# Optimization experiments

Measured on AMD Instinct MI355X. Metric: run time of the kernel, lower is better.

Reference implementation:

```python
import jax, jax.numpy as jnp
import numpy as np

EPS = 1e-5

def instance_norm(x):
    # x: [B, C, H, W]; normalize over spatial dims per (b, c), no affine
    mean = jnp.mean(x, axis=(2, 3), keepdims=True)
    var = jnp.var(x, axis=(2, 3), keepdims=True)
    return (x - mean) * jax.lax.rsqrt(var + EPS)

def conv1x1(x, w, b):
    # x: [B, Cin, H, W], w: [Cout, Cin], b: [Cout]
    return jnp.einsum('bchw,oc->bohw', x, w) + b[None, :, None, None]

def setup_inputs() -> dict:
    key = jax.random.key(0)
    k1, k2, k3 = jax.random.split(key, 3)
    B, Cin, Cout, H, W = 16, 256, 256, 128, 128
    x = jax.random.normal(k1, (B, Cin, H, W), dtype=jnp.float32)
    # PyTorch Conv2d init: U(-s, s), s = 1/sqrt(fan_in) with fan_in = Cin*1*1
    s1 = 1.0 / np.sqrt(Cin)
    w1 = jax.random.uniform(k2, (Cout, Cin), jnp.float32, -s1, s1)
    b1 = jax.random.uniform(jax.random.fold_in(k2, 1), (Cout,), jnp.float32, -s1, s1)
    s2 = 1.0 / np.sqrt(Cout)
    w2 = jax.random.uniform(k3, (Cout, Cout), jnp.float32, -s2, s2)
    b2 = jax.random.uniform(jax.random.fold_in(k3, 1), (Cout,), jnp.float32, -s2, s2)
    return {"x": x, "w1": w1, "b1": b1, "w2": w2, "b2": b2}

def reference(x, w1, b1, w2, b2):
    h = jax.nn.relu(conv1x1(instance_norm(x), w1, b1))
    out = jax.nn.relu(conv1x1(instance_norm(h), w2, b2))
    return out
```

## Files before the change

### kernel.cpp

```cpp
#include <hip/hip_runtime.h>
#include <hip/hip_bf16.h>
#include <cstdint>
#include <cstddef>

#define DEVI __device__ __forceinline__

typedef unsigned short u16;
using frag_ab = __attribute__((ext_vector_type(8))) short;
using f32x4   = __attribute__((ext_vector_type(4))) float;

constexpr int HW = 16384;
constexpr int NC = 256;

DEVI u16 bf16bits(float f) {
    union { float f; uint32_t u; } cv; cv.f = f;
    uint32_t u = cv.u;
    u += 0x7fffu + ((u >> 16) & 1u);
    return (u16)(u >> 16);
}

DEVI void gload16(const void* g, void* l) {
    __builtin_amdgcn_global_load_lds(
        (const __attribute__((address_space(1))) uint32_t*)g,
        (__attribute__((address_space(3))) uint32_t*)l, 16, 0, 0);
}

DEVI frag_ab read_frag(const u16* slab, int row, int l4) {
    const int phys = (l4 ^ row ^ (row >> 2)) & 3;
    return *(const frag_ab*)((const char*)slab + row * 64 + phys * 16);
}

__global__ __launch_bounds__(256) void transpose_stats_kernel(
    const float* __restrict__ x, u16* __restrict__ xt,
    float* __restrict__ ps, float* __restrict__ pq)
{
    constexpr int PADW = 68;
    __shared__ __align__(16) u16 tile[64 * PADW];
    const int b = blockIdx.z, c0 = blockIdx.y * 64, p0 = blockIdx.x * 64;
    const int pblk = blockIdx.x;
    const int t = threadIdx.x;
    const int lane = t & 63, w = t >> 6;
    const int pq_ = lane & 15, cq = lane >> 4;
    const int quad = w * 4 + cq;
    const float* xb = x + ((size_t)b * NC + c0) * HW + p0;

    float va[4][4];
    float aS[4], aQ[4];
    #pragma unroll
    for (int j = 0; j < 4; ++j) {
        const float4 v = *(const float4*)(xb + (size_t)(quad * 4 + j) * HW + pq_ * 4);
        va[j][0] = v.x; va[j][1] = v.y; va[j][2] = v.z; va[j][3] = v.w;
        float s1 = v.x + v.y + v.z + v.w;
        float s2 = v.x*v.x + v.y*v.y + v.z*v.z + v.w*v.w;
        #pragma unroll
        for (int d = 1; d < 16; d <<= 1) {
            s1 += __shfl_xor(s1, d, 64);
            s2 += __shfl_xor(s2, d, 64);
        }
        aS[j] = s1; aQ[j] = s2;
    }
    if (pq_ == 0) {
        const float4 vs = {aS[0], aS[1], aS[2], aS[3]};
        const float4 vq = {aQ[0], aQ[1], aQ[2], aQ[3]};
        *(float4*)&ps[((size_t)b * 256 + pblk) * NC + c0 + quad * 4] = vs;
        *(float4*)&pq[((size_t)b * 256 + pblk) * NC + c0 + quad * 4] = vq;
    }
    #pragma unroll
    for (int i = 0; i < 4; ++i) {
        alignas(8) u16 pk[4];
        #pragma unroll
        for (int j = 0; j < 4; ++j) pk[j] = bf16bits(va[j][i]);
        *(uint2*)&tile[(pq_ * 4 + i) * PADW + quad * 4] = *(const uint2*)pk;
    }
    __syncthreads();
    const int pl = t >> 2, q = t & 3;
    u16* dst = xt + ((size_t)b * HW + p0 + pl) * NC + c0;
    #pragma unroll
    for (int s = 0; s < 2; ++s) {
        const int ch8 = q + s * 4;
        const uint2 lo = *(const uint2*)&tile[pl * PADW + ch8 * 8];
        const uint2 hi = *(const uint2*)&tile[pl * PADW + ch8 * 8 + 4];
        const uint4 o4 = {lo.x, lo.y, hi.x, hi.y};
        *(uint4*)(dst + ch8 * 8) = o4;
    }
}

__global__ __launch_bounds__(256) void fold_kernel(
    const float* __restrict__ w, const float* __restrict__ bias,
    const float* __restrict__ ps, const float* __restrict__ pq,
    u16* __restrict__ we, float* __restrict__ be)
{
    const int b = blockIdx.y, oc = blockIdx.x * 64;
    __shared__ float mu[NC], rs[NC];
    __shared__ __align__(16) float wt[64 * NC];
    const int t = threadIdx.x;
    {
        float s1 = 0.f, s2 = 0.f;
        const float* pp = ps + (size_t)b * 256 * NC + t;
        const float* qq = pq + (size_t)b * 256 * NC + t;
        for (int i = 0; i < 256; ++i) {
            s1 += pp[(size_t)i * NC];
            s2 += qq[(size_t)i * NC];
        }
        const float m = s1 * (1.0f / HW);
        mu[t] = m;
        rs[t] = rsqrtf(s2 * (1.0f / HW) - m * m + 1e-5f);
    }
    #pragma unroll
    for (int i = 0; i < 16; ++i)
        *(float4*)&wt[i*1024 + t*4] = *(const float4*)&w[(size_t)oc*NC + i*1024 + t*4];
    __syncthreads();
    const int o = oc + (t >> 2), q = t & 3;
    const float* wrow = &wt[(t >> 2) * NC];
    u16* werow = we + ((size_t)b * NC + o) * NC;
    float bacc = 0.f;
    for (int cc = 0; cc < 8; ++cc) {
        alignas(16) u16 pk[8];
        #pragma unroll
        for (int jj = 0; jj < 8; ++jj) {
            const int c = q*64 + cc*8 + jj;
            const float wv = wrow[c];
            bacc -= wv * mu[c] * rs[c];
            pk[jj] = bf16bits(wv * rs[c]);
        }
        *(uint4*)(werow + q*64 + cc*8) = *(const uint4*)pk;
    }
    bacc += __shfl_xor(bacc, 1, 64);
    bacc += __shfl_xor(bacc, 2, 64);
    if (q == 0) be[b*NC + o] = bias[o] + bacc;
}

template<int STAGE>
__global__ __launch_bounds__(256, 2) void gemm_kernel(
    const u16* __restrict__ pixM,
    const u16* __restrict__ wMat,
    const float* __restrict__ biasE,
    u16* __restrict__ outB,
    float* __restrict__ outF,
    float* __restrict__ hps, float* __restrict__ hpq)
{
    __shared__ __align__(16) u16 ldsP[8 * 64 * 32];
    __shared__ __align__(16) u16 ldsW[2][256 * 32];

    const int b = blockIdx.y, pblk = blockIdx.x;
    const int p0 = pblk * 64;
    const int tid = threadIdx.x;
    const int lane = tid & 63, wid = tid >> 6;
    const int l15 = lane & 15, l4 = lane >> 4;

    const u16* gP = pixM + ((size_t)b * HW + p0) * NC;
    const u16* gW = wMat + (size_t)b * NC * NC;

    const int rin  = lane >> 2;
    const int prow = wid * 16 + rin;
    const int psl  = ((lane & 3) ^ prow ^ (prow >> 2)) & 3;
    int wrowq[4], wslq[4];
    #pragma unroll
    for (int q = 0; q < 4; ++q) {
        wrowq[q] = wid * 64 + q * 16 + rin;
        wslq[q]  = ((lane & 3) ^ wrowq[q] ^ (wrowq[q] >> 2)) & 3;
    }

    #pragma unroll
    for (int ks = 0; ks < 8; ++ks)
        gload16(gP + (size_t)prow * NC + ks * 32 + psl * 8,
                (char*)ldsP + ks * 4096 + wid * 1024);
    #pragma unroll
    for (int q = 0; q < 4; ++q)
        gload16(gW + (size_t)wrowq[q] * NC + wslq[q] * 8,
                (char*)ldsW[0] + (wid * 4 + q) * 1024);

    f32x4 acc[4][4];
    #pragma unroll
    for (int i = 0; i < 4; ++i)
        #pragma unroll
        for (int j = 0; j < 4; ++j)
            acc[i][j] = (f32x4){0.f, 0.f, 0.f, 0.f};

    for (int ks = 0; ks < 8; ++ks) {
        asm volatile("s_waitcnt vmcnt(0)" ::: "memory");
        __builtin_amdgcn_s_barrier();

        const u16* wslab = ldsW[ks & 1];
        const u16* pslab = ldsP + ks * 2048;

        const u16* sA; const u16* sB; int aOff, bOff;
        if constexpr (STAGE == 1) { sA = pslab; aOff = 0;        sB = wslab; bOff = wid * 64; }
        else                      { sA = wslab; aOff = wid * 64; sB = pslab; bOff = 0; }

        frag_ab a[4], bf[4];
        #pragma unroll
        for (int mi = 0; mi < 4; ++mi)
            a[mi] = read_frag(sA, aOff + 16*mi + l15, l4);
        #pragma unroll
        for (int ni = 0; ni < 4; ++ni)
            bf[ni] = read_frag(sB, bOff + 16*ni + l15, l4);

        if (ks < 7) {
            const int k0 = (ks + 1) * 32;
            #pragma unroll
            for (int q = 0; q < 4; ++q)
                gload16(gW + (size_t)wrowq[q] * NC + k0 + wslq[q] * 8,
                        (char*)ldsW[(ks + 1) & 1] + (wid * 4 + q) * 1024);
        }

        #pragma unroll
        for (int ni = 0; ni < 4; ++ni)
            #pragma unroll
            for (int mi = 0; mi < 4; ++mi)
                acc[mi][ni] = __builtin_amdgcn_mfma_f32_16x16x32_bf16(a[mi], bf[ni], acc[mi][ni], 0, 0, 0);
    }

    if constexpr (STAGE == 1) {
        u16* htp = outB + ((size_t)b * HW + p0) * NC + wid * 64;
        float s1[4] = {0.f,0.f,0.f,0.f}, s2[4] = {0.f,0.f,0.f,0.f};
        #pragma unroll
        for (int ni = 0; ni < 4; ++ni) {
            const float bn = biasE[b*NC + wid*64 + 16*ni + l15];
            #pragma unroll
            for (int mi = 0; mi < 4; ++mi) {
                #pragma unroll
                for (int r = 0; r < 4; ++r) {
                    const float v = fmaxf(acc[mi][ni][r] + bn, 0.f);
                    s1[ni] += v; s2[ni] += v * v;
                    htp[(size_t)(16*mi + l4*4 + r) * NC + 16*ni + l15] = bf16bits(v);
                }
            }
        }
        #pragma unroll
        for (int ni = 0; ni < 4; ++ni) {
            float a1 = s1[ni], a2 = s2[ni];
            a1 += __shfl_xor(a1, 16, 64); a1 += __shfl_xor(a1, 32, 64);
            a2 += __shfl_xor(a2, 16, 64); a2 += __shfl_xor(a2, 32, 64);
            if (l4 == 0) {
                const int col = wid*64 + 16*ni + l15;
                hps[((size_t)b * 256 + pblk) * NC + col] = a1;
                hpq[((size_t)b * 256 + pblk) * NC + col] = a2;
            }
        }
    } else {
        float* op = outF + ((size_t)b * NC + wid * 64) * HW + p0;
        #pragma unroll
        for (int mi = 0; mi < 4; ++mi) {
            #pragma unroll
            for (int r = 0; r < 4; ++r) {
                const int orow = 16*mi + l4*4 + r;
                const float bm = biasE[b*NC + wid*64 + orow];
                #pragma unroll
                for (int ni = 0; ni < 4; ++ni)
                    op[(size_t)orow * HW + 16*ni + l15] = fmaxf(acc[mi][ni][r] + bm, 0.f);
            }
        }
    }
}

extern "C" void kernel_launch(void* const* d_in, const int* in_sizes, int n_in,
                              void* d_out, int out_size, void* d_ws, size_t ws_size,
                              hipStream_t stream)
{
    (void)in_sizes; (void)n_in; (void)out_size;
    const float* x  = (const float*)d_in[0];
    const float* w1 = (const float*)d_in[1];
    const float* b1 = (const float*)d_in[2];
    const float* w2 = (const float*)d_in[3];
    const float* b2 = (const float*)d_in[4];
    float* out = (float*)d_out;

    char* od = (char*)d_out;
    u16*   xt  = (u16*)od;
    float* xps = (float*)(od + 134217728);
    float* xpq = (float*)(od + 138412032);
    float* hps = (float*)(od + 142606336);
    float* hpq = (float*)(od + 146800640);

    char* ws = (char*)d_ws;
    const size_t NEED = 138444800;
    if (ws_size < NEED) return;
    u16*   ht  = (u16*)(ws);
    u16*   w1e = (u16*)(ws + 134217728);
    u16*   w2e = (u16*)(ws + 136314880);
    float* b1e = (float*)(ws + 138412032);
    float* b2e = (float*)(ws + 138428416);

    transpose_stats_kernel<<<dim3(HW/64, NC/64, 16), 256, 0, stream>>>(x, xt, xps, xpq);
    fold_kernel<<<dim3(4, 16), 256, 0, stream>>>(w1, b1, xps, xpq, w1e, b1e);
    gemm_kernel<1><<<dim3(HW/64, 16), 256, 0, stream>>>(xt, w1e, b1e, ht, nullptr, hps, hpq);
    fold_kernel<<<dim3(4, 16), 256, 0, stream>>>(w2, b2, hps, hpq, w2e, b2e);
    gemm_kernel<2><<<dim3(HW/64, 16), 256, 0, stream>>>(ht, w2e, b2e, nullptr, out, nullptr, nullptr);
}
```

Before: 315.8 us.

## Load weight fragments directly to registers, drop LDS weight buffer, add nontemporal stores

```diff
diff --git a/kernel.cpp b/kernel.cpp
--- a/kernel.cpp
+++ b/kernel.cpp
@@ -8,6 +8,7 @@
 typedef unsigned short u16;
 using frag_ab = __attribute__((ext_vector_type(8))) short;
 using f32x4   = __attribute__((ext_vector_type(4))) float;
+using u32x4   = __attribute__((ext_vector_type(4))) unsigned int;
 
 constexpr int HW = 16384;
 constexpr int NC = 256;
@@ -80,8 +81,8 @@
         const int ch8 = q + s * 4;
         const uint2 lo = *(const uint2*)&tile[pl * PADW + ch8 * 8];
         const uint2 hi = *(const uint2*)&tile[pl * PADW + ch8 * 8 + 4];
-        const uint4 o4 = {lo.x, lo.y, hi.x, hi.y};
-        *(uint4*)(dst + ch8 * 8) = o4;
+        const u32x4 o4 = {lo.x, lo.y, hi.x, hi.y};
+        __builtin_nontemporal_store(o4, (u32x4*)(dst + ch8 * 8));
     }
 }
 
@@ -131,7 +132,7 @@
 }
 
 template<int STAGE>
-__global__ __launch_bounds__(256, 2) void gemm_kernel(
+__global__ __launch_bounds__(256, 3) void gemm_kernel(
     const u16* __restrict__ pixM,
     const u16* __restrict__ wMat,
     const float* __restrict__ biasE,
@@ -140,7 +141,6 @@
     float* __restrict__ hps, float* __restrict__ hpq)
 {
     __shared__ __align__(16) u16 ldsP[8 * 64 * 32];
-    __shared__ __align__(16) u16 ldsW[2][256 * 32];
 
     const int b = blockIdx.y, pblk = blockIdx.x;
     const int p0 = pblk * 64;
@@ -154,21 +154,13 @@
     const int rin  = lane >> 2;
     const int prow = wid * 16 + rin;
     const int psl  = ((lane & 3) ^ prow ^ (prow >> 2)) & 3;
-    int wrowq[4], wslq[4];
-    #pragma unroll
-    for (int q = 0; q < 4; ++q) {
-        wrowq[q] = wid * 64 + q * 16 + rin;
-        wslq[q]  = ((lane & 3) ^ wrowq[q] ^ (wrowq[q] >> 2)) & 3;
-    }
 
     #pragma unroll
     for (int ks = 0; ks < 8; ++ks)
         gload16(gP + (size_t)prow * NC + ks * 32 + psl * 8,
                 (char*)ldsP + ks * 4096 + wid * 1024);
-    #pragma unroll
-    for (int q = 0; q < 4; ++q)
-        gload16(gW + (size_t)wrowq[q] * NC + wslq[q] * 8,
-                (char*)ldsW[0] + (wid * 4 + q) * 1024);
+
+    const u16* wbase = gW + (size_t)(wid * 64 + l15) * NC + l4 * 8;
 
     f32x4 acc[4][4];
     #pragma unroll
@@ -177,38 +169,37 @@
         for (int j = 0; j < 4; ++j)
             acc[i][j] = (f32x4){0.f, 0.f, 0.f, 0.f};
 
+    frag_ab wf[2][4];
+    #pragma unroll
+    for (int f = 0; f < 4; ++f)
+        wf[0][f] = *(const frag_ab*)(wbase + (size_t)f * 16 * NC);
+
+    asm volatile("s_waitcnt vmcnt(0)" ::: "memory");
+    __builtin_amdgcn_s_barrier();
+
+    #pragma unroll
     for (int ks = 0; ks < 8; ++ks) {
-        asm volatile("s_waitcnt vmcnt(0)" ::: "memory");
-        __builtin_amdgcn_s_barrier();
-
-        const u16* wslab = ldsW[ks & 1];
+        const int cur = ks & 1;
+        if (ks < 7) {
+            #pragma unroll
+            for (int f = 0; f < 4; ++f)
+                wf[cur ^ 1][f] = *(const frag_ab*)(wbase + (size_t)f * 16 * NC + (ks + 1) * 32);
+        }
         const u16* pslab = ldsP + ks * 2048;
-
-        const u16* sA; const u16* sB; int aOff, bOff;
-        if constexpr (STAGE == 1) { sA = pslab; aOff = 0;        sB = wslab; bOff = wid * 64; }
-        else                      { sA = wslab; aOff = wid * 64; sB = pslab; bOff = 0; }
-
-        frag_ab a[4], bf[4];
-        #pragma unroll
-        for (int mi = 0; mi < 4; ++mi)
-            a[mi] = read_frag(sA, aOff + 16*mi + l15, l4);
+        frag_ab pf[4];
+        #pragma unroll
+        for (int f = 0; f < 4; ++f)
+            pf[f] = read_frag(pslab, 16 * f + l15, l4);
+
         #pragma unroll
         for (int ni = 0; ni < 4; ++ni)
-            bf[ni] = read_frag(sB, bOff + 16*ni + l15, l4);
-
-        if (ks < 7) {
-            const int k0 = (ks + 1) * 32;
-            #pragma unroll
-            for (int q = 0; q < 4; ++q)
-                gload16(gW + (size_t)wrowq[q] * NC + k0 + wslq[q] * 8,
-                        (char*)ldsW[(ks + 1) & 1] + (wid * 4 + q) * 1024);
-        }
-
-        #pragma unroll
-        for (int ni = 0; ni < 4; ++ni)
-            #pragma unroll
-            for (int mi = 0; mi < 4; ++mi)
-                acc[mi][ni] = __builtin_amdgcn_mfma_f32_16x16x32_bf16(a[mi], bf[ni], acc[mi][ni], 0, 0, 0);
+            #pragma unroll
+            for (int mi = 0; mi < 4; ++mi) {
+                if constexpr (STAGE == 1)
+                    acc[mi][ni] = __builtin_amdgcn_mfma_f32_16x16x32_bf16(pf[mi], wf[cur][ni], acc[mi][ni], 0, 0, 0);
+                else
+                    acc[mi][ni] = __builtin_amdgcn_mfma_f32_16x16x32_bf16(wf[cur][mi], pf[ni], acc[mi][ni], 0, 0, 0);
+            }
     }
 
     if constexpr (STAGE == 1) {
@@ -223,7 +214,8 @@
                 for (int r = 0; r < 4; ++r) {
                     const float v = fmaxf(acc[mi][ni][r] + bn, 0.f);
                     s1[ni] += v; s2[ni] += v * v;
-                    htp[(size_t)(16*mi + l4*4 + r) * NC + 16*ni + l15] = bf16bits(v);
+                    __builtin_nontemporal_store(bf16bits(v),
+                        htp + (size_t)(16*mi + l4*4 + r) * NC + 16*ni + l15);
                 }
             }
         }
@@ -248,7 +240,8 @@
                 const float bm = biasE[b*NC + wid*64 + orow];
                 #pragma unroll
                 for (int ni = 0; ni < 4; ++ni)
-                    op[(size_t)orow * HW + 16*ni + l15] = fmaxf(acc[mi][ni][r] + bm, 0.f);
+                    __builtin_nontemporal_store(fmaxf(acc[mi][ni][r] + bm, 0.f),
+                        op + (size_t)orow * HW + 16*ni + l15);
             }
         }
     }
```

Measured after the change: 416.7 us. +31.9%, slower.

## Triple-buffer weight slabs, drop per-step barriers, and vectorize GEMM epilogue stores

Applied to the files above, without the earlier changes.

```diff
diff --git a/kernel.cpp b/kernel.cpp
--- a/kernel.cpp
+++ b/kernel.cpp
@@ -140,7 +140,7 @@
     float* __restrict__ hps, float* __restrict__ hpq)
 {
     __shared__ __align__(16) u16 ldsP[8 * 64 * 32];
-    __shared__ __align__(16) u16 ldsW[2][256 * 32];
+    __shared__ __align__(16) u16 ldsW[3][256 * 32];
 
     const int b = blockIdx.y, pblk = blockIdx.x;
     const int p0 = pblk * 64;
@@ -161,14 +161,20 @@
         wslq[q]  = ((lane & 3) ^ wrowq[q] ^ (wrowq[q] >> 2)) & 3;
     }
 
+    auto stageW = [&](int ks, int buf) {
+        const int k0 = ks * 32;
+        #pragma unroll
+        for (int q = 0; q < 4; ++q)
+            gload16(gW + (size_t)wrowq[q] * NC + k0 + wslq[q] * 8,
+                    (char*)ldsW[buf] + (wid * 4 + q) * 1024);
+    };
+
     #pragma unroll
     for (int ks = 0; ks < 8; ++ks)
         gload16(gP + (size_t)prow * NC + ks * 32 + psl * 8,
                 (char*)ldsP + ks * 4096 + wid * 1024);
-    #pragma unroll
-    for (int q = 0; q < 4; ++q)
-        gload16(gW + (size_t)wrowq[q] * NC + wslq[q] * 8,
-                (char*)ldsW[0] + (wid * 4 + q) * 1024);
+    stageW(0, 0);
+    stageW(1, 1);
 
     f32x4 acc[4][4];
     #pragma unroll
@@ -177,78 +183,106 @@
         for (int j = 0; j < 4; ++j)
             acc[i][j] = (f32x4){0.f, 0.f, 0.f, 0.f};
 
+    asm volatile("s_waitcnt vmcnt(4)" ::: "memory");
+    __builtin_amdgcn_s_barrier();
+
+    #pragma unroll
     for (int ks = 0; ks < 8; ++ks) {
-        asm volatile("s_waitcnt vmcnt(0)" ::: "memory");
-        __builtin_amdgcn_s_barrier();
-
-        const u16* wslab = ldsW[ks & 1];
+        if (ks >= 1) {
+            if (ks < 7) asm volatile("s_waitcnt vmcnt(4)" ::: "memory");
+            else        asm volatile("s_waitcnt vmcnt(0)" ::: "memory");
+        }
+        const u16* wslab = ldsW[ks % 3];
         const u16* pslab = ldsP + ks * 2048;
 
-        const u16* sA; const u16* sB; int aOff, bOff;
-        if constexpr (STAGE == 1) { sA = pslab; aOff = 0;        sB = wslab; bOff = wid * 64; }
-        else                      { sA = wslab; aOff = wid * 64; sB = pslab; bOff = 0; }
-
-        frag_ab a[4], bf[4];
+        frag_ab a[4], bfr[4];
+        if constexpr (STAGE == 1) {
+            #pragma unroll
+            for (int f = 0; f < 4; ++f) a[f]   = read_frag(wslab, wid * 64 + 16*f + l15, l4);
+            #pragma unroll
+            for (int f = 0; f < 4; ++f) bfr[f] = read_frag(pslab, 16*f + l15, l4);
+        } else {
+            #pragma unroll
+            for (int f = 0; f < 4; ++f) a[f]   = read_frag(pslab, 16*f + l15, l4);
+            #pragma unroll
+            for (int f = 0; f < 4; ++f) bfr[f] = read_frag(wslab, wid * 64 + 16*f + l15, l4);
+        }
+
+        #pragma unroll
+        for (int ni = 0; ni < 4; ++ni)
+            #pragma unroll
+            for (int mi = 0; mi < 4; ++mi)
+                acc[mi][ni] = __builtin_amdgcn_mfma_f32_16x16x32_bf16(a[mi], bfr[ni], acc[mi][ni], 0, 0, 0);
+
+        if (ks + 2 < 8) {
+            asm volatile("s_waitcnt lgkmcnt(0)" ::: "memory");
+            stageW(ks + 2, (ks + 2) % 3);
+        }
+    }
+
+    if constexpr (STAGE == 1) {
+        u16* htbase = outB + ((size_t)b * HW + p0) * NC + wid * 64;
+        float4 vb[4];
         #pragma unroll
         for (int mi = 0; mi < 4; ++mi)
-            a[mi] = read_frag(sA, aOff + 16*mi + l15, l4);
-        #pragma unroll
-        for (int ni = 0; ni < 4; ++ni)
-            bf[ni] = read_frag(sB, bOff + 16*ni + l15, l4);
-
-        if (ks < 7) {
-            const int k0 = (ks + 1) * 32;
-            #pragma unroll
-            for (int q = 0; q < 4; ++q)
-                gload16(gW + (size_t)wrowq[q] * NC + k0 + wslq[q] * 8,
-                        (char*)ldsW[(ks + 1) & 1] + (wid * 4 + q) * 1024);
-        }
-
-        #pragma unroll
-        for (int ni = 0; ni < 4; ++ni)
-            #pragma unroll
-            for (int mi = 0; mi < 4; ++mi)
-                acc[mi][ni] = __builtin_amdgcn_mfma_f32_16x16x32_bf16(a[mi], bf[ni], acc[mi][ni], 0, 0, 0);
-    }
-
-    if constexpr (STAGE == 1) {
-        u16* htp = outB + ((size_t)b * HW + p0) * NC + wid * 64;
-        float s1[4] = {0.f,0.f,0.f,0.f}, s2[4] = {0.f,0.f,0.f,0.f};
+            vb[mi] = *(const float4*)&biasE[b*NC + wid*64 + 16*mi + l4*4];
+        float s1v[4][4], s2v[4][4];
+        #pragma unroll
+        for (int mi = 0; mi < 4; ++mi)
+            #pragma unroll
+            for (int r = 0; r < 4; ++r) { s1v[mi][r] = 0.f; s2v[mi][r] = 0.f; }
+
         #pragma unroll
         for (int ni = 0; ni < 4; ++ni) {
-            const float bn = biasE[b*NC + wid*64 + 16*ni + l15];
+            u16* rowp = htbase + (size_t)(16*ni + l15) * NC;
             #pragma unroll
             for (int mi = 0; mi < 4; ++mi) {
+                alignas(8) u16 pk[4];
+                const float bx[4] = {vb[mi].x, vb[mi].y, vb[mi].z, vb[mi].w};
                 #pragma unroll
                 for (int r = 0; r < 4; ++r) {
-                    const float v = fmaxf(acc[mi][ni][r] + bn, 0.f);
-                    s1[ni] += v; s2[ni] += v * v;
-                    htp[(size_t)(16*mi + l4*4 + r) * NC + 16*ni + l15] = bf16bits(v);
+                    const float v = fmaxf(acc[mi][ni][r] + bx[r], 0.f);
+                    s1v[mi][r] += v; s2v[mi][r] += v * v;
+                    pk[r] = bf16bits(v);
                 }
+                *(uint2*)&rowp[16*mi + l4*4] = *(const uint2*)pk;
             }
         }
         #pragma unroll
+        for (int mi = 0; mi < 4; ++mi)
+            #pragma unroll
+            for (int r = 0; r < 4; ++r) {
+                float a1 = s1v[mi][r], a2 = s2v[mi][r];
+                #pragma unroll
+                for (int d = 1; d < 16; d <<= 1) {
+                    a1 += __shfl_xor(a1, d, 64);
+                    a2 += __shfl_xor(a2, d, 64);
+                }
+                s1v[mi][r] = a1; s2v[mi][r] = a2;
+            }
+        if (l15 == 0) {
+            #pragma unroll
+            for (int mi = 0; mi < 4; ++mi) {
+                const int o = wid*64 + 16*mi + l4*4;
+                const float4 w1 = {s1v[mi][0], s1v[mi][1], s1v[mi][2], s1v[mi][3]};
+                const float4 w2 = {s2v[mi][0], s2v[mi][1], s2v[mi][2], s2v[mi][3]};
+                *(float4*)&hps[((size_t)b * 256 + pblk) * NC + o] = w1;
+                *(float4*)&hpq[((size_t)b * 256 + pblk) * NC + o] = w2;
+            }
+        }
+    } else {
+        #pragma unroll
         for (int ni = 0; ni < 4; ++ni) {
-            float a1 = s1[ni], a2 = s2[ni];
-            a1 += __shfl_xor(a1, 16, 64); a1 += __shfl_xor(a1, 32, 64);
-            a2 += __shfl_xor(a2, 16, 64); a2 += __shfl_xor(a2, 32, 64);
-            if (l4 == 0) {
-                const int col = wid*64 + 16*ni + l15;
-                hps[((size_t)b * 256 + pblk) * NC + col] = a1;
-                hpq[((size_t)b * 256 + pblk) * NC + col] = a2;
-            }
-        }
-    } else {
-        float* op = outF + ((size_t)b * NC + wid * 64) * HW + p0;
-        #pragma unroll
-        for (int mi = 0; mi < 4; ++mi) {
-            #pragma unroll
-            for (int r = 0; r < 4; ++r) {
-                const int orow = 16*mi + l4*4 + r;
-                const float bm = biasE[b*NC + wid*64 + orow];
-                #pragma unroll
-                for (int ni = 0; ni < 4; ++ni)
-                    op[(size_t)orow * HW + 16*ni + l15] = fmaxf(acc[mi][ni][r] + bm, 0.f);
+            const int o = wid*64 + 16*ni + l15;
+            const float bm = biasE[b*NC + o];
+            float* colp = outF + ((size_t)b * NC + o) * HW + p0;
+            #pragma unroll
+            for (int mi = 0; mi < 4; ++mi) {
+                const float4 v = {fmaxf(acc[mi][ni][0] + bm, 0.f),
+                                  fmaxf(acc[mi][ni][1] + bm, 0.f),
+                                  fmaxf(acc[mi][ni][2] + bm, 0.f),
+                                  fmaxf(acc[mi][ni][3] + bm, 0.f)};
+                *(float4*)&colp[16*mi + l4*4] = v;
             }
         }
     }
```

Result: slower. 337.8 us (+7.0%).
